# Performance work log

Measured on AMD Instinct MI355X. Metric: run time of the kernel, lower is better.

Reference implementation:

```python
import jax, jax.numpy as jnp
import numpy as np

# ---- model hyperparams (from init_kwargs) ----
N_USERS = 200000
N_ITEMS = 100000
DIM = 64
NNZ = 3000000
BATCH = 4096
N_HOPS = 3          # context_hops
EPS = 0.1           # SimGCL perturbation magnitude
TEMP = 0.2          # tau
CL_RATE = 0.5       # lamb
DECAY = 1e-4        # l2


def setup_inputs() -> dict:
    key = jax.random.key(0)
    k = jax.random.split(key, 8)
    user_embed = (jax.random.normal(k[0], (N_USERS, DIM), dtype=jnp.float32) * 0.01)
    item_embed = (jax.random.normal(k[1], (N_ITEMS, DIM), dtype=jnp.float32) * 0.01)
    N = N_USERS + N_ITEMS
    # COO normalized adjacency (buffer, not a parameter in the torch module)
    adj_rows = jax.random.randint(k[2], (NNZ,), 0, N)
    adj_cols = jax.random.randint(k[3], (NNZ,), 0, N)
    adj_vals = jax.random.uniform(k[4], (NNZ,), dtype=jnp.float32) * 0.2
    # unique index batches (torch code calls torch.unique for the CL loss;
    # sampling without replacement makes skipping unique exact, since the
    # InfoNCE mean is permutation invariant)
    users = jax.random.permutation(k[5], N_USERS)[:BATCH].astype(jnp.int32)
    pos_items = jax.random.permutation(k[6], N_ITEMS)[:BATCH].astype(jnp.int32)
    neg_items = jax.random.randint(k[7], (BATCH,), 0, N_ITEMS)
    return {"user_embed": user_embed, "item_embed": item_embed,
            "adj_vals": adj_vals, "adj_rows": adj_rows, "adj_cols": adj_cols,
            "users": users, "pos_items": pos_items, "neg_items": neg_items}


def _spmm(vals, rows, cols, x):
    # torch.sparse.mm(A, x) with A in COO form: out[r] += v * x[c]
    return jax.ops.segment_sum(vals[:, None] * x[cols], rows, num_segments=x.shape[0])


def _gcn(user_embed, item_embed, vals, rows, cols, perturbed, key):
    ego = jnp.concatenate([user_embed, item_embed], axis=0)  # [N, D]
    acc = jnp.zeros_like(ego)
    for h in range(N_HOPS):
        ego = _spmm(vals, rows, cols, ego)
        if perturbed:
            noise = jax.random.uniform(jax.random.fold_in(key, h), ego.shape, dtype=ego.dtype)
            noise = noise / jnp.maximum(jnp.linalg.norm(noise, axis=-1, keepdims=True), 1e-12)
            ego = ego + jnp.sign(ego) * noise * EPS
        acc = acc + ego
    mean = acc / N_HOPS   # stack + mean over hops == running-sum / n_hops
    return mean[:N_USERS], mean[N_USERS:]


def _info_nce(v1, v2, temp):
    v1 = v1 / jnp.maximum(jnp.linalg.norm(v1, axis=1, keepdims=True), 1e-12)
    v2 = v2 / jnp.maximum(jnp.linalg.norm(v2, axis=1, keepdims=True), 1e-12)
    pos = jnp.exp(jnp.sum(v1 * v2, axis=-1) / temp)              # [B]
    ttl = jnp.sum(jnp.exp((v1 @ v2.T) / temp), axis=1)           # [B]
    return jnp.mean(-jnp.log(pos / ttl + 1e-5))


def reference(user_embed, item_embed, adj_vals, adj_rows, adj_cols, users, pos_items, neg_items):
    # --- recommendation branch (no perturbation) ---
    ru, ri = _gcn(user_embed, item_embed, adj_vals, adj_rows, adj_cols, False, jax.random.key(0))
    ue, pe, ne = ru[users], ri[pos_items], ri[neg_items]
    pos_score = jnp.sum(ue * pe, axis=1)
    neg_score = jnp.sum(ue * ne, axis=1)
    rec_loss = jnp.mean(-jnp.log(1e-5 + jax.nn.sigmoid(pos_score - neg_score)))
    reg_loss = DECAY * (jnp.linalg.norm(ue) + jnp.linalg.norm(pe))  # Frobenius norms
    # --- contrastive branch: two perturbed views of the whole GCN ---
    u1, i1 = _gcn(user_embed, item_embed, adj_vals, adj_rows, adj_cols, True, jax.random.key(101))
    u2, i2 = _gcn(user_embed, item_embed, adj_vals, adj_rows, adj_cols, True, jax.random.key(202))
    cl_loss = CL_RATE * (_info_nce(u1[users], u2[users], TEMP)
                         + _info_nce(i1[pos_items], i2[pos_items], TEMP))
    return rec_loss + reg_loss + cl_loss
```

## Files before the change

kernel.cpp:

```cpp
#include <hip/hip_runtime.h>
#include <stdint.h>

#define NUSERS  200000
#define NITEMS  100000
#define NTOT    300000
#define DIM     64
#define NU64    (NUSERS * DIM)
#define NNZC    3000000
#define BATCH   4096
#define B64     (BATCH * DIM)
#define EPSP    0.1f
#define INV_TEMP 5.0f
#define SCAN_ELEMS 1024
#define GELEMS ((size_t)7 * B64 + 2 * BATCH + 8)
#define BCAP   163840

#define BSHIFT 11
#define BROWS  (1 << BSHIFT)
#define NB     ((NTOT + BROWS - 1) / BROWS)
#define CHUNK  4096
#define NCHUNK ((NNZC + CHUNK - 1) / CHUNK)
#define NH     (NB * NCHUNK)
#define CASTB  ((NTOT * DIM) / 2048)
#define Z4V    (NTOT / 4)
#define Z4T    ((2 * BATCH + 8) / 4)
#define ZVB    ((Z4V + 511) / 512)
#define ZTB    ((Z4T + 511) / 512)
#define SCB    ((NTOT + 255) / 256)

typedef short bf16x8 __attribute__((ext_vector_type(8)));
typedef float f32x4  __attribute__((ext_vector_type(4)));

__device__ __forceinline__ float b2f(unsigned short h) {
  return __uint_as_float(((uint32_t)h) << 16);
}
__device__ __forceinline__ unsigned short f2b(float f) {
  uint32_t b = __float_as_uint(f);
  uint32_t r = b + 0x7FFFu + ((b >> 16) & 1u);
  return (unsigned short)(r >> 16);
}

__device__ __forceinline__ uint32_t mix32(uint32_t h) {
  h ^= h >> 16; h *= 0x85EBCA6Bu;
  h ^= h >> 13; h *= 0xC2B2AE35u;
  h ^= h >> 16;
  return h;
}
__device__ __forceinline__ uint32_t noise_key(uint32_t seed, uint32_t hop) {
  return mix32(seed * 0x9E3779B9u + hop * 0x85EBCA6Bu + 0x1BD11BDAu);
}
__device__ __forceinline__ float fast_unif(uint32_t key, uint32_t e) {
  uint32_t h = mix32(key + e * 0x9E3779B9u);
  return __uint_as_float((h >> 9) | 0x3F800000u) - 1.0f;
}
__device__ __forceinline__ float n_ss4(uint32_t key, uint32_t rq, float4& u) {
  uint32_t h = mix32(key + rq * 0x9E3779B9u);
  u.x = ((float)(h & 255u)         + 0.5f) * (1.0f / 256.0f);
  u.y = ((float)((h >> 8) & 255u)  + 0.5f) * (1.0f / 256.0f);
  u.z = ((float)((h >> 16) & 255u) + 0.5f) * (1.0f / 256.0f);
  u.w = ((float)(h >> 24)          + 0.5f) * (1.0f / 256.0f);
  return u.x * u.x + u.y * u.y + u.z * u.z + u.w * u.w;
}

__device__ __forceinline__ float sgnf(float a) {
  return (a > 0.f) ? 1.f : ((a < 0.f) ? -1.f : 0.f);
}

__global__ __launch_bounds__(256) void partA_cast(
    const int* __restrict__ rows, int* __restrict__ Hcnt,
    const float* __restrict__ uemb, const float* __restrict__ iemb,
    unsigned short* __restrict__ X0,
    int* __restrict__ vflag, float* __restrict__ ttlz,
    float* __restrict__ sc1, float* __restrict__ sc2) {
  int blk = blockIdx.x;
  if (blk >= NCHUNK + CASTB + ZVB + ZTB) {
    int r = (blk - (NCHUNK + CASTB + ZVB + ZTB)) * 256 + threadIdx.x;
    if (r >= NTOT) return;
    const uint32_t k101 = noise_key(101u, 0u);
    const uint32_t k202 = noise_key(202u, 0u);
    float s1 = 0.f, s2 = 0.f;
    for (int q = 0; q < 16; ++q) {
      float4 u;
      s1 += n_ss4(k101, (uint32_t)(r * 16 + q), u);
      s2 += n_ss4(k202, (uint32_t)(r * 16 + q), u);
    }
    sc1[r] = EPSP / fmaxf(sqrtf(s1), 1e-12f);
    sc2[r] = EPSP / fmaxf(sqrtf(s2), 1e-12f);
    return;
  }
  if (blk >= NCHUNK + CASTB + ZVB) {
    int i4 = (blk - NCHUNK - CASTB - ZVB) * 512 + threadIdx.x;
    float4 z = make_float4(0.f, 0.f, 0.f, 0.f);
    if (i4 < Z4T) ((float4*)ttlz)[i4] = z;
    i4 += 256;
    if (i4 < Z4T) ((float4*)ttlz)[i4] = z;
    return;
  }
  if (blk >= NCHUNK + CASTB) {
    int i4 = (blk - NCHUNK - CASTB) * 512 + threadIdx.x;
    int4 z = make_int4(0, 0, 0, 0);
    if (i4 < Z4V) ((int4*)vflag)[i4] = z;
    i4 += 256;
    if (i4 < Z4V) ((int4*)vflag)[i4] = z;
    return;
  }
  if (blk >= NCHUNK) {
    int base = (blk - NCHUNK) * 2048 + threadIdx.x * 8;
    const float* src = (base < NU64) ? (uemb + base) : (iemb + (base - NU64));
    float4 f0 = ((const float4*)src)[0];
    float4 f1 = ((const float4*)src)[1];
    uint4 o;
    o.x = ((uint32_t)f2b(f0.y) << 16) | f2b(f0.x);
    o.y = ((uint32_t)f2b(f0.w) << 16) | f2b(f0.z);
    o.z = ((uint32_t)f2b(f1.y) << 16) | f2b(f1.x);
    o.w = ((uint32_t)f2b(f1.w) << 16) | f2b(f1.z);
    *(uint4*)(X0 + base) = o;
    return;
  }
  __shared__ int bc[256];
  int c = blk, t = threadIdx.x;
  bc[t] = 0;
  __syncthreads();
  int base = c * CHUNK;
  for (int i = t; i < CHUNK; i += 256) {
    int e = base + i;
    if (e < NNZC) atomicAdd(&bc[rows[e] >> BSHIFT], 1);
  }
  __syncthreads();
  if (t < NB) Hcnt[t * NCHUNK + c] = bc[t];
}

__global__ void scan_block(const int* __restrict__ cnt, int* __restrict__ out,
                           int* __restrict__ bsums, int n) {
  __shared__ int tmp[SCAN_ELEMS];
  int base = blockIdx.x * SCAN_ELEMS;
  int t = threadIdx.x;
  #pragma unroll
  for (int q = 0; q < 4; ++q) {
    int k = t + q * 256, i = base + k;
    tmp[k] = (i < n) ? cnt[i] : 0;
  }
  __syncthreads();
  for (int off = 1; off < SCAN_ELEMS; off <<= 1) {
    int v[4];
    #pragma unroll
    for (int q = 0; q < 4; ++q) {
      int k = t + q * 256;
      v[q] = (k >= off) ? tmp[k - off] : 0;
    }
    __syncthreads();
    #pragma unroll
    for (int q = 0; q < 4; ++q) tmp[t + q * 256] += v[q];
    __syncthreads();
  }
  #pragma unroll
  for (int q = 0; q < 4; ++q) {
    int k = t + q * 256, i = base + k;
    if (i < n) out[i] = (k == 0) ? 0 : tmp[k - 1];
  }
  if (t == 0) bsums[blockIdx.x] = tmp[SCAN_ELEMS - 1];
}

__global__ void add_offsets_scan(int* __restrict__ out,
                                 const int* __restrict__ bsums,
                                 int n, int nb) {
  __shared__ int tmp[512];
  int t = threadIdx.x;
  tmp[t] = (t < nb) ? bsums[t] : 0;
  tmp[t + 256] = (t + 256 < nb) ? bsums[t + 256] : 0;
  __syncthreads();
  for (int off = 1; off < 512; off <<= 1) {
    int v0 = (t >= off) ? tmp[t - off] : 0;
    int v1 = (t + 256 >= off) ? tmp[t + 256 - off] : 0;
    __syncthreads();
    tmp[t] += v0; tmp[t + 256] += v1;
    __syncthreads();
  }
  int i = blockIdx.x * 256 + t;
  if (i < n) {
    int b = i >> 10;
    out[i] += (b == 0) ? 0 : tmp[b - 1];
  }
}

__global__ void add_offsets_emit_scan(int* __restrict__ vmap,
                                      const int* __restrict__ bsums,
                                      const int* __restrict__ vflag,
                                      int* __restrict__ vlist,
                                      int* __restrict__ nV, int nb) {
  __shared__ int tmp[512];
  int t = threadIdx.x;
  tmp[t] = (t < nb) ? bsums[t] : 0;
  tmp[t + 256] = (t + 256 < nb) ? bsums[t + 256] : 0;
  __syncthreads();
  for (int off = 1; off < 512; off <<= 1) {
    int v0 = (t >= off) ? tmp[t - off] : 0;
    int v1 = (t + 256 >= off) ? tmp[t + 256 - off] : 0;
    __syncthreads();
    tmp[t] += v0; tmp[t + 256] += v1;
    __syncthreads();
  }
  int i = blockIdx.x * 256 + t;
  if (i >= NTOT) return;
  int b = i >> 10;
  int m = vmap[i] + ((b == 0) ? 0 : tmp[b - 1]);
  vmap[i] = m;
  if (vflag[i] && m < BCAP) vlist[m] = i;
  if (i == NTOT - 1) {
    int tot = m + vflag[i];
    nV[0] = (tot > BCAP) ? BCAP : tot;
  }
}

__global__ __launch_bounds__(256) void partB(const float* __restrict__ vals,
                                             const int* __restrict__ rows,
                                             const int* __restrict__ cols,
                                             const int* __restrict__ Hofs,
                                             int2* __restrict__ midp,
                                             int* __restrict__ midr) {
  __shared__ int2 stv[CHUNK];
  __shared__ int  str_[CHUNK];
  __shared__ int  cnt[256];
  __shared__ int  sc[256];
  __shared__ int  adj[NB];
  int c = blockIdx.x, t = threadIdx.x;
  cnt[t] = 0;
  __syncthreads();
  int base = c * CHUNK;
  for (int i = t; i < CHUNK; i += 256) {
    int e = base + i;
    if (e < NNZC) atomicAdd(&cnt[rows[e] >> BSHIFT], 1);
  }
  __syncthreads();
  sc[t] = cnt[t];
  __syncthreads();
  for (int off = 1; off < 256; off <<= 1) {
    int u = (t >= off) ? sc[t - off] : 0;
    __syncthreads();
    sc[t] += u;
    __syncthreads();
  }
  int excl = sc[t] - cnt[t];
  cnt[t] = excl;
  if (t < NB) adj[t] = Hofs[t * NCHUNK + c] - excl;
  __syncthreads();
  for (int i = t; i < CHUNK; i += 256) {
    int e = base + i;
    if (e < NNZC) {
      int r = rows[e];
      int b = r >> BSHIFT;
      int p = atomicAdd(&cnt[b], 1);
      stv[p] = make_int2(__float_as_int(vals[e]), cols[e] * DIM);
      str_[p] = r;
    }
  }
  __syncthreads();
  int n = NNZC - base;
  if (n > CHUNK) n = CHUNK;
  for (int p = t; p < n; p += 256) {
    int r = str_[p];
    int b = r >> BSHIFT;
    int dst = adj[b] + p;
    midp[dst] = stv[p];
    midr[dst] = r;
  }
}

__global__ __launch_bounds__(256) void partC(const int2* __restrict__ midp,
                                             const int* __restrict__ midr,
                                             const int* __restrict__ Hofs,
                                             int* __restrict__ rs,
                                             int2* __restrict__ pairs) {
  __shared__ int h[BROWS];
  __shared__ int tsum[256];
  int b = blockIdx.x, t = threadIdx.x;
  int row0 = b << BSHIFT;
  for (int i = t; i < BROWS; i += 256) h[i] = 0;
  __syncthreads();
  int s = Hofs[b * NCHUNK];
  int e = (b + 1 < NB) ? Hofs[(b + 1) * NCHUNK] : NNZC;
  for (int p = s + t; p < e; p += 256)
    atomicAdd(&h[midr[p] - row0], 1);
  __syncthreads();
  int loc[8], run = 0;
  #pragma unroll
  for (int k = 0; k < 8; ++k) { loc[k] = run; run += h[t * 8 + k]; }
  tsum[t] = run;
  __syncthreads();
  for (int off = 1; off < 256; off <<= 1) {
    int v = (t >= off) ? tsum[t - off] : 0;
    __syncthreads();
    tsum[t] += v;
    __syncthreads();
  }
  int baseT = (t == 0) ? 0 : tsum[t - 1];
  #pragma unroll
  for (int k = 0; k < 8; ++k) {
    int i = t * 8 + k;
    int pos = s + baseT + loc[k];
    if (row0 + i < NTOT) rs[row0 + i] = pos;
    h[i] = pos;
  }
  if (b == NB - 1 && t == 0) rs[NTOT] = NNZC;
  __syncthreads();
  for (int p = s + t; p < e; p += 256) {
    int r = midr[p];
    int2 v = midp[p];
    int pos = atomicAdd(&h[r - row0], 1);
    pairs[pos] = v;
  }
}

__global__ __launch_bounds__(256) void mark_v(const int* __restrict__ u,
                                              const int* __restrict__ p,
                                              const int* __restrict__ n,
                                              const int* __restrict__ rs,
                                              const int2* __restrict__ pairs,
                                              int* __restrict__ vflag) {
  int i = blockIdx.x * 256 + threadIdx.x;
  if (i >= 3 * BATCH) return;
  int v = (i < BATCH) ? u[i]
        : (i < 2 * BATCH) ? (NUSERS + p[i - BATCH])
        : (NUSERS + n[i - 2 * BATCH]);
  vflag[v] = 1;
  int s = rs[v], e = rs[v + 1];
  for (int j = s; j < e; ++j) vflag[(unsigned)pairs[j].y >> 6] = 1;
}

__global__ __launch_bounds__(256) void spmm_hop0(
    const int2* __restrict__ pairs, const int* __restrict__ rs,
    const unsigned short* __restrict__ x,
    unsigned short* __restrict__ y) {
  int tid  = threadIdx.x;
  int lane = tid & 63;
  int q    = lane & 15;
  int wave = (blockIdx.x * 256 + tid) >> 6;
  int r    = wave * 4 + (lane >> 4);
  int s    = rs[r];
  int e    = rs[r + 1];
  int q4 = q * 4;
  float a0[4] = {0.f, 0.f, 0.f, 0.f};
  for (int j = s; j < e; j += 8) {
    int2 p[8];
    #pragma unroll
    for (int k = 0; k < 8; ++k)
      p[k] = (j + k < e) ? pairs[j + k] : make_int2(0, 0);
    #pragma unroll
    for (int k = 0; k < 8; ++k) {
      float v = __int_as_float(p[k].x);
      unsigned o = (unsigned)(p[k].y + q4);
      ushort4 h = *(const ushort4*)(x + o);
      a0[0] = fmaf(v, b2f(h.x), a0[0]); a0[1] = fmaf(v, b2f(h.y), a0[1]);
      a0[2] = fmaf(v, b2f(h.z), a0[2]); a0[3] = fmaf(v, b2f(h.w), a0[3]);
    }
  }
  int ebase = r * 64 + q4;
  ushort4 st;
  st.x = f2b(a0[0]); st.y = f2b(a0[1]); st.z = f2b(a0[2]); st.w = f2b(a0[3]);
  *(ushort4*)(y + ebase) = st;
}

__global__ __launch_bounds__(256) void spmm_subz(
    const int2* __restrict__ pairs, const int* __restrict__ rs,
    const int* __restrict__ vlist, const int* __restrict__ nVp,
    const unsigned short* __restrict__ A,
    const float* __restrict__ sc1, const float* __restrict__ sc2,
    unsigned short* __restrict__ y0, unsigned short* __restrict__ y1,
    unsigned short* __restrict__ y2) {
  int nV = nVp[0];
  int z  = blockIdx.x % 3;
  int bx = blockIdx.x / 3;
  if (bx * 16 >= nV) return;
  unsigned short* y = (z == 0) ? y0 : ((z == 1) ? y1 : y2);
  const float* scg = (z == 1) ? sc1 : sc2;
  int tid  = threadIdx.x;
  int lane = tid & 63;
  int q    = lane & 15;
  int wave = (bx * 256 + tid) >> 6;
  int slot = wave * 4 + (lane >> 4);
  if (slot >= nV) return;
  int v = vlist[slot];
  int s = rs[v];
  int e = rs[v + 1];
  int q4 = q * 4;
  float a0[4] = {0.f, 0.f, 0.f, 0.f};
  if (z == 0) {
    for (int j = s; j < e; j += 8) {
      int2 p[8];
      #pragma unroll
      for (int k = 0; k < 8; ++k)
        p[k] = (j + k < e) ? pairs[j + k] : make_int2(0, 0);
      #pragma unroll
      for (int k = 0; k < 8; ++k) {
        float vv = __int_as_float(p[k].x);
        unsigned o = (unsigned)(p[k].y + q4);
        ushort4 h = *(const ushort4*)(A + o);
        a0[0] = fmaf(vv, b2f(h.x), a0[0]); a0[1] = fmaf(vv, b2f(h.y), a0[1]);
        a0[2] = fmaf(vv, b2f(h.z), a0[2]); a0[3] = fmaf(vv, b2f(h.w), a0[3]);
      }
    }
  } else {
    const uint32_t kg = noise_key((z == 1) ? 101u : 202u, 0u);
    for (int j = s; j < e; j += 8) {
      int2 p[8];
      #pragma unroll
      for (int k = 0; k < 8; ++k)
        p[k] = (j + k < e) ? pairs[j + k] : make_int2(0, 0);
      #pragma unroll
      for (int k = 0; k < 8; ++k) {
        float vv = __int_as_float(p[k].x);
        unsigned o = (unsigned)(p[k].y + q4);
        ushort4 h = *(const ushort4*)(A + o);
        float sc = scg[(unsigned)p[k].y >> 6];
        float4 u;
        n_ss4(kg, ((unsigned)p[k].y >> 2) + (unsigned)q, u);
        float a_ = b2f(h.x), b_ = b2f(h.y), c_ = b2f(h.z), d_ = b2f(h.w);
        a0[0] = fmaf(vv, fmaf(sgnf(a_) * u.x, sc, a_), a0[0]);
        a0[1] = fmaf(vv, fmaf(sgnf(b_) * u.y, sc, b_), a0[1]);
        a0[2] = fmaf(vv, fmaf(sgnf(c_) * u.z, sc, c_), a0[2]);
        a0[3] = fmaf(vv, fmaf(sgnf(d_) * u.w, sc, d_), a0[3]);
      }
    }
    uint32_t key = noise_key((z == 1) ? 101u : 202u, 1u);
    int en = v * 64 + q4;
    float u[4], ss = 0.f;
    #pragma unroll
    for (int k = 0; k < 4; ++k) {
      u[k] = fast_unif(key, (uint32_t)(en + k));
      ss += u[k] * u[k];
    }
    #pragma unroll
    for (int msk = 1; msk < 16; msk <<= 1) ss += __shfl_xor(ss, msk);
    float sc = EPSP / fmaxf(sqrtf(ss), 1e-12f);
    #pragma unroll
    for (int k = 0; k < 4; ++k) a0[k] += sgnf(a0[k]) * u[k] * sc;
  }
  ushort4 st;
  st.x = f2b(a0[0]); st.y = f2b(a0[1]); st.z = f2b(a0[2]); st.w = f2b(a0[3]);
  *(ushort4*)(y + slot * 64 + q4) = st;
}

__global__ __launch_bounds__(256) void hop2g7(
    const int2* __restrict__ pairs, const int* __restrict__ rs,
    const unsigned short* __restrict__ Abuf,
    const unsigned short* __restrict__ B0,
    const unsigned short* __restrict__ B1,
    const unsigned short* __restrict__ B2,
    const int* __restrict__ vmap,
    const float* __restrict__ sc1, const float* __restrict__ sc2,
    const int* __restrict__ users, const int* __restrict__ pos,
    const int* __restrict__ neg,
    float* __restrict__ g, unsigned short* __restrict__ gb) {
  int by = blockIdx.y;
  int br = (by < 3) ? 0 : ((by < 5) ? 1 : 2);
  const int* idx = (by == 2) ? neg
                 : ((by == 1 || by == 4 || by == 6) ? pos : users);
  int base = (by == 0 || by == 3 || by == 5) ? 0 : NUSERS;
  float* o = g + (size_t)by * B64;
  const unsigned short* Bt = (br == 0) ? B0 : ((br == 1) ? B1 : B2);
  uint32_t seed = (br == 1) ? 101u : 202u;
  int tid  = threadIdx.x;
  int lane = tid & 63;
  int q    = lane & 15;
  int q4 = q * 4;
  int slot = blockIdx.x * 16 + (tid >> 6) * 4 + (lane >> 4);
  int row  = base + idx[slot];
  int s    = rs[row];
  int e    = rs[row + 1];
  float a0[4] = {0.f, 0.f, 0.f, 0.f};
  for (int j = s; j < e; j += 8) {
    int2 p[8];
    #pragma unroll
    for (int k = 0; k < 8; ++k)
      p[k] = (j + k < e) ? pairs[j + k] : make_int2(0, 0);
    int sl[8];
    #pragma unroll
    for (int k = 0; k < 8; ++k)
      sl[k] = vmap[(unsigned)p[k].y >> 6];
    #pragma unroll
    for (int k = 0; k < 8; ++k) {
      float v = __int_as_float(p[k].x);
      unsigned of = (unsigned)(sl[k] * DIM + q4);
      ushort4 h = *(const ushort4*)(Bt + of);
      a0[0] = fmaf(v, b2f(h.x), a0[0]); a0[1] = fmaf(v, b2f(h.y), a0[1]);
      a0[2] = fmaf(v, b2f(h.z), a0[2]); a0[3] = fmaf(v, b2f(h.w), a0[3]);
    }
  }
  if (br) {
    uint32_t key = noise_key(seed, 2u);
    int en = row * 64 + q4;
    float u[4], ss = 0.f;
    #pragma unroll
    for (int k = 0; k < 4; ++k) {
      u[k] = fast_unif(key, (uint32_t)(en + k));
      ss += u[k] * u[k];
    }
    #pragma unroll
    for (int msk = 1; msk < 16; msk <<= 1) ss += __shfl_xor(ss, msk);
    float sc = EPSP / fmaxf(sqrtf(ss), 1e-12f);
    #pragma unroll
    for (int k = 0; k < 4; ++k) a0[k] += sgnf(a0[k]) * u[k] * sc;
  }
  size_t rbA = (size_t)row * DIM + q4;
  size_t rbB = (size_t)vmap[row] * DIM + q4;
  ushort4 ha = *(const ushort4*)(Abuf + rbA);
  ushort4 hb = *(const ushort4*)(Bt + rbB);
  float af[4] = {b2f(ha.x), b2f(ha.y), b2f(ha.z), b2f(ha.w)};
  if (br) {
    uint32_t key0 = noise_key(seed, 0u);
    float scn = ((br == 1) ? sc1 : sc2)[row];
    float4 u;
    n_ss4(key0, (uint32_t)(row * 16 + q), u);
    af[0] = fmaf(sgnf(af[0]) * u.x, scn, af[0]);
    af[1] = fmaf(sgnf(af[1]) * u.y, scn, af[1]);
    af[2] = fmaf(sgnf(af[2]) * u.z, scn, af[2]);
    af[3] = fmaf(sgnf(af[3]) * u.w, scn, af[3]);
  }
  float rv[4];
  rv[0] = (af[0] + b2f(hb.x)) + a0[0];
  rv[1] = (af[1] + b2f(hb.y)) + a0[1];
  rv[2] = (af[2] + b2f(hb.z)) + a0[2];
  rv[3] = (af[3] + b2f(hb.w)) + a0[3];
  if (br) {
    float ss = rv[0]*rv[0] + rv[1]*rv[1] + rv[2]*rv[2] + rv[3]*rv[3];
    #pragma unroll
    for (int msk = 1; msk < 16; msk <<= 1) ss += __shfl_xor(ss, msk);
    float inv = 1.0f / fmaxf(sqrtf(ss), 1e-12f);
    #pragma unroll
    for (int k = 0; k < 4; ++k) rv[k] *= inv;
  }
  int og = slot * 64 + q4;
  *(float4*)(o + og) = make_float4(rv[0], rv[1], rv[2], rv[3]);
  if (br) {
    unsigned short* ob = gb + (size_t)(by - 3) * B64;
    ushort4 sb;
    sb.x = f2b(rv[0]); sb.y = f2b(rv[1]); sb.z = f2b(rv[2]); sb.w = f2b(rv[3]);
    *(ushort4*)(ob + og) = sb;
  }
}

__global__ __launch_bounds__(256) void nce_ttl_mfma(
    const unsigned short* __restrict__ u1b, const unsigned short* __restrict__ u2b,
    float* __restrict__ tu,
    const unsigned short* __restrict__ w1b, const unsigned short* __restrict__ w2b,
    float* __restrict__ tw) {
  const unsigned short* V1 = (blockIdx.z == 0) ? u1b : w1b;
  const unsigned short* V2 = (blockIdx.z == 0) ? u2b : w2b;
  float* ttl = (blockIdx.z == 0) ? tu : tw;
  int tid  = threadIdx.x;
  int lane = tid & 63;
  int wv   = tid >> 6;
  int lr   = lane & 15;
  int lk   = (lane >> 4) * 8;
  int m0   = blockIdx.x * 64 + wv * 16;
  bf16x8 a0 = *(const bf16x8*)(V1 + (size_t)(m0 + lr) * DIM + lk);
  bf16x8 a1 = *(const bf16x8*)(V1 + (size_t)(m0 + lr) * DIM + 32 + lk);
  float rowsum[4] = {0.f, 0.f, 0.f, 0.f};
  int n0 = blockIdx.y * 256;
  for (int ch = 0; ch < 4; ++ch) {
    int nc = n0 + ch * 64;
    #pragma unroll
    for (int nt = 0; nt < 4; ++nt) {
      int col = nc + nt * 16 + lr;
      bf16x8 b0 = *(const bf16x8*)(V2 + (size_t)col * DIM + lk);
      bf16x8 b1 = *(const bf16x8*)(V2 + (size_t)col * DIM + 32 + lk);
      f32x4 c = {0.f, 0.f, 0.f, 0.f};
      c = __builtin_amdgcn_mfma_f32_16x16x32_bf16(a0, b0, c, 0, 0, 0);
      c = __builtin_amdgcn_mfma_f32_16x16x32_bf16(a1, b1, c, 0, 0, 0);
      #pragma unroll
      for (int rr = 0; rr < 4; ++rr)
        rowsum[rr] += __expf(c[rr] * INV_TEMP);
    }
  }
  #pragma unroll
  for (int rr = 0; rr < 4; ++rr) {
    float s = rowsum[rr];
    #pragma unroll
    for (int m = 1; m < 16; m <<= 1) s += __shfl_xor(s, m);
    rowsum[rr] = s;
  }
  if (lr == 0) {
    int rbase = m0 + (lane >> 4) * 4;
    #pragma unroll
    for (int rr = 0; rr < 4; ++rr)
      atomicAdd(&ttl[rbase + rr], rowsum[rr]);
  }
}

__global__ __launch_bounds__(256) void loss3(const float* __restrict__ g,
                                             const float* __restrict__ ttl_u,
                                             float* __restrict__ acc) {
  __shared__ float red[3][4];
  int role = blockIdx.y;
  int tid = threadIdx.x, lane = tid & 63, wv = tid >> 6;
  int gw = blockIdx.x * 4 + wv;
  if (role == 0) {
    const float* ue = g;
    const float* pe = g + (size_t)B64;
    const float* ne = g + 2 * (size_t)B64;
    const float third = 1.0f / 3.0f;
    float l = 0.f, su = 0.f, sp = 0.f;
    for (int r = gw; r < BATCH; r += 256) {
      int gid = r * 64 + lane;
      float u = ue[gid] * third, p = pe[gid] * third, n = ne[gid] * third;
      float ps = u * p, ns = u * n;
      su += u * u; sp += p * p;
      #pragma unroll
      for (int m = 32; m; m >>= 1) { ps += __shfl_xor(ps, m); ns += __shfl_xor(ns, m); }
      if (lane == 0) {
        float sig = 1.0f / (1.0f + __expf(-(ps - ns)));
        l += -logf(1e-5f + sig);
      }
    }
    #pragma unroll
    for (int m = 32; m; m >>= 1) { su += __shfl_xor(su, m); sp += __shfl_xor(sp, m); }
    if (lane == 0) { red[0][wv] = l; red[1][wv] = su; red[2][wv] = sp; }
    __syncthreads();
    if (tid == 0) {
      atomicAdd(acc + 0, red[0][0] + red[0][1] + red[0][2] + red[0][3]);
      atomicAdd(acc + 1, red[1][0] + red[1][1] + red[1][2] + red[1][3]);
      atomicAdd(acc + 2, red[2][0] + red[2][1] + red[2][2] + red[2][3]);
    }
  } else {
    int by = role - 1;
    const float* v1 = g + (size_t)(3 + by) * B64;
    const float* v2 = g + (size_t)(5 + by) * B64;
    const float* ttl = ttl_u + by * BATCH;
    float l = 0.f;
    for (int r = gw; r < BATCH; r += 256) {
      int gid = r * 64 + lane;
      float p = v1[gid] * v2[gid];
      #pragma unroll
      for (int m = 32; m; m >>= 1) p += __shfl_xor(p, m);
      if (lane == 0) l += -logf(__expf(p * INV_TEMP) / ttl[r] + 1e-5f);
    }
    if (lane == 0) red[0][wv] = l;
    __syncthreads();
    if (tid == 0)
      atomicAdd(acc + 3 + by, red[0][0] + red[0][1] + red[0][2] + red[0][3]);
  }
}

__global__ void finalize_kernel(const float* __restrict__ acc, float* __restrict__ out) {
  out[0] = acc[0] * (1.0f / BATCH)
         + 1e-4f * (sqrtf(acc[1]) + sqrtf(acc[2]))
         + 0.5f * (acc[3] + acc[4]) * (1.0f / BATCH);
}

extern "C" void kernel_launch(void* const* d_in, const int* in_sizes, int n_in,
                              void* d_out, int out_size, void* d_ws, size_t ws_size,
                              hipStream_t stream) {
  (void)in_sizes; (void)n_in; (void)out_size; (void)ws_size;
  const float* user_embed = (const float*)d_in[0];
  const float* item_embed = (const float*)d_in[1];
  const float* adj_vals   = (const float*)d_in[2];
  const int*   adj_rows   = (const int*)d_in[3];
  const int*   adj_cols   = (const int*)d_in[4];
  const int*   users      = (const int*)d_in[5];
  const int*   pos_items  = (const int*)d_in[6];
  const int*   neg_items  = (const int*)d_in[7];
  float* out = (float*)d_out;

  const size_t bufElems = (size_t)NTOT * DIM;
  const size_t bcapE    = (size_t)BCAP * DIM;

  unsigned short* A  = (unsigned short*)d_ws;
  unsigned short* B0 = A + bufElems;
  unsigned short* B1 = B0 + bcapE;
  unsigned short* B2 = B1 + bcapE;
  float* sc1 = (float*)(B2 + bcapE);
  float* sc2 = sc1 + NTOT;
  int2*  pairs = (int2*)(sc2 + NTOT);
  float* g     = (float*)(pairs + NNZC);
  int*   rs    = (int*)(g + GELEMS);
  int*   bsums = rs + (NTOT + 4);
  int*   vflag = bsums + 512;
  int*   vmap  = vflag + NTOT;
  int*   vlist = vmap + NTOT;
  int*   nVd   = vlist + NTOT;
  unsigned short* gb =
      (unsigned short*)(((uintptr_t)(nVd + 1) + 31) & ~(uintptr_t)31);

  float* ttl_u = g + 7 * (size_t)B64;
  float* ttl_i = ttl_u + BATCH;
  float* acc   = ttl_u + 2 * BATCH;
  unsigned short* g_u1b = gb + 0 * (size_t)B64;
  unsigned short* g_i1b = gb + 1 * (size_t)B64;
  unsigned short* g_u2b = gb + 2 * (size_t)B64;
  unsigned short* g_i2b = gb + 3 * (size_t)B64;

  int2* midp = (int2*)A;
  int*  midr = (int*)(midp + NNZC);
  int*  Hcnt = midr + NNZC;
  int*  Hofs = Hcnt + NH;
  unsigned short* X0 = B0;

  partA_cast<<<NCHUNK + CASTB + ZVB + ZTB + SCB, 256, 0, stream>>>(
      adj_rows, Hcnt, user_embed, item_embed, X0, vflag, ttl_u, sc1, sc2);
  const int nhb = (NH + SCAN_ELEMS - 1) / SCAN_ELEMS;
  scan_block<<<nhb, 256, 0, stream>>>(Hcnt, Hofs, bsums, NH);
  add_offsets_scan<<<(NH + 255) / 256, 256, 0, stream>>>(Hofs, bsums, NH, nhb);
  partB<<<NCHUNK, 256, 0, stream>>>(adj_vals, adj_rows, adj_cols, Hofs, midp, midr);
  partC<<<NB, 256, 0, stream>>>(midp, midr, Hofs, rs, pairs);

  mark_v<<<(3 * BATCH + 255) / 256, 256, 0, stream>>>(
      users, pos_items, neg_items, rs, pairs, vflag);
  const int nvb = (NTOT + SCAN_ELEMS - 1) / SCAN_ELEMS;
  scan_block<<<nvb, 256, 0, stream>>>(vflag, vmap, bsums, NTOT);
  add_offsets_emit_scan<<<(NTOT + 255) / 256, 256, 0, stream>>>(
      vmap, bsums, vflag, vlist, nVd, nvb);

  const int spmm_blocks = NTOT / 16;

  spmm_hop0<<<spmm_blocks, 256, 0, stream>>>(pairs, rs, X0, A);

  spmm_subz<<<3 * spmm_blocks, 256, 0, stream>>>(
      pairs, rs, vlist, nVd, A, sc1, sc2, B0, B1, B2);

  dim3 h2g7(BATCH / 16, 7);
  hop2g7<<<h2g7, 256, 0, stream>>>(pairs, rs, A, B0, B1, B2, vmap, sc1, sc2,
                                   users, pos_items, neg_items, g, gb);

  dim3 nce_grid(BATCH / 64, BATCH / 256, 2);
  nce_ttl_mfma<<<nce_grid, 256, 0, stream>>>(g_u1b, g_u2b, ttl_u,
                                             g_i1b, g_i2b, ttl_i);
  dim3 lgrid(64, 3);
  loss3<<<lgrid, 256, 0, stream>>>(g, ttl_u, acc);
  finalize_kernel<<<1, 1, 0, stream>>>(acc, out);
}
```

Measured before the change: 528.9 us.

## Precompute perturbed hop-1 views in hop0 and fuse three views per gather

The first-hop SpMM now also writes the two noise-perturbed copies of its output, with the noise norm computed by in-row shuffles, so the separate per-row norm-scale pass and the per-edge noise regeneration in hop 2 are removed. The hop-2 and hop-3 kernels then accumulate all three views in one pass over each row's edge list, sharing the index and value loads instead of launching a separate block set per view. The cost is two extra full-size bf16 buffers written and then gathered from at random, which adds memory traffic and register pressure.

```diff
diff --git a/kernel.cpp b/kernel.cpp
--- a/kernel.cpp
+++ b/kernel.cpp
@@ -26,7 +26,6 @@
 #define Z4T    ((2 * BATCH + 8) / 4)
 #define ZVB    ((Z4V + 511) / 512)
 #define ZTB    ((Z4T + 511) / 512)
-#define SCB    ((NTOT + 255) / 256)
 
 typedef short bf16x8 __attribute__((ext_vector_type(8)));
 typedef float f32x4  __attribute__((ext_vector_type(4)));
@@ -70,24 +69,8 @@
     const int* __restrict__ rows, int* __restrict__ Hcnt,
     const float* __restrict__ uemb, const float* __restrict__ iemb,
     unsigned short* __restrict__ X0,
-    int* __restrict__ vflag, float* __restrict__ ttlz,
-    float* __restrict__ sc1, float* __restrict__ sc2) {
+    int* __restrict__ vflag, float* __restrict__ ttlz) {
   int blk = blockIdx.x;
-  if (blk >= NCHUNK + CASTB + ZVB + ZTB) {
-    int r = (blk - (NCHUNK + CASTB + ZVB + ZTB)) * 256 + threadIdx.x;
-    if (r >= NTOT) return;
-    const uint32_t k101 = noise_key(101u, 0u);
-    const uint32_t k202 = noise_key(202u, 0u);
-    float s1 = 0.f, s2 = 0.f;
-    for (int q = 0; q < 16; ++q) {
-      float4 u;
-      s1 += n_ss4(k101, (uint32_t)(r * 16 + q), u);
-      s2 += n_ss4(k202, (uint32_t)(r * 16 + q), u);
-    }
-    sc1[r] = EPSP / fmaxf(sqrtf(s1), 1e-12f);
-    sc2[r] = EPSP / fmaxf(sqrtf(s2), 1e-12f);
-    return;
-  }
   if (blk >= NCHUNK + CASTB + ZVB) {
     int i4 = (blk - NCHUNK - CASTB - ZVB) * 512 + threadIdx.x;
     float4 z = make_float4(0.f, 0.f, 0.f, 0.f);
@@ -327,10 +310,13 @@
   for (int j = s; j < e; ++j) vflag[(unsigned)pairs[j].y >> 6] = 1;
 }
 
-__global__ __launch_bounds__(256) void spmm_hop0(
+__global__ __launch_bounds__(256) void spmm_hop3(
     const int2* __restrict__ pairs, const int* __restrict__ rs,
     const unsigned short* __restrict__ x,
-    unsigned short* __restrict__ y) {
+    unsigned short* __restrict__ A, unsigned short* __restrict__ A1,
+    unsigned short* __restrict__ A2) {
+  const uint32_t k101 = noise_key(101u, 0u);
+  const uint32_t k202 = noise_key(202u, 0u);
   int tid  = threadIdx.x;
   int lane = tid & 63;
   int q    = lane & 15;
@@ -357,72 +343,82 @@
   int ebase = r * 64 + q4;
   ushort4 st;
   st.x = f2b(a0[0]); st.y = f2b(a0[1]); st.z = f2b(a0[2]); st.w = f2b(a0[3]);
-  *(ushort4*)(y + ebase) = st;
-}
-
-__global__ __launch_bounds__(256) void spmm_subz(
+  *(ushort4*)(A + ebase) = st;
+  float a[4] = {b2f(st.x), b2f(st.y), b2f(st.z), b2f(st.w)};
+  float4 u1, u2;
+  float s1 = n_ss4(k101, (uint32_t)(r * 16 + q), u1);
+  float s2 = n_ss4(k202, (uint32_t)(r * 16 + q), u2);
+  #pragma unroll
+  for (int m = 1; m < 16; m <<= 1) {
+    s1 += __shfl_xor(s1, m);
+    s2 += __shfl_xor(s2, m);
+  }
+  float sc1 = EPSP / fmaxf(sqrtf(s1), 1e-12f);
+  float sc2 = EPSP / fmaxf(sqrtf(s2), 1e-12f);
+  float g0 = sgnf(a[0]), g1 = sgnf(a[1]), g2 = sgnf(a[2]), g3 = sgnf(a[3]);
+  ushort4 o1, o2;
+  o1.x = f2b(fmaf(g0 * u1.x, sc1, a[0]));
+  o1.y = f2b(fmaf(g1 * u1.y, sc1, a[1]));
+  o1.z = f2b(fmaf(g2 * u1.z, sc1, a[2]));
+  o1.w = f2b(fmaf(g3 * u1.w, sc1, a[3]));
+  o2.x = f2b(fmaf(g0 * u2.x, sc2, a[0]));
+  o2.y = f2b(fmaf(g1 * u2.y, sc2, a[1]));
+  o2.z = f2b(fmaf(g2 * u2.z, sc2, a[2]));
+  o2.w = f2b(fmaf(g3 * u2.w, sc2, a[3]));
+  *(ushort4*)(A1 + ebase) = o1;
+  *(ushort4*)(A2 + ebase) = o2;
+}
+
+__global__ __launch_bounds__(256) void spmm_sub3t(
     const int2* __restrict__ pairs, const int* __restrict__ rs,
     const int* __restrict__ vlist, const int* __restrict__ nVp,
     const unsigned short* __restrict__ A,
-    const float* __restrict__ sc1, const float* __restrict__ sc2,
+    const unsigned short* __restrict__ A1,
+    const unsigned short* __restrict__ A2,
     unsigned short* __restrict__ y0, unsigned short* __restrict__ y1,
     unsigned short* __restrict__ y2) {
   int nV = nVp[0];
-  int z  = blockIdx.x % 3;
-  int bx = blockIdx.x / 3;
-  if (bx * 16 >= nV) return;
-  unsigned short* y = (z == 0) ? y0 : ((z == 1) ? y1 : y2);
-  const float* scg = (z == 1) ? sc1 : sc2;
+  if (blockIdx.x * 16 >= nV) return;
   int tid  = threadIdx.x;
   int lane = tid & 63;
   int q    = lane & 15;
-  int wave = (bx * 256 + tid) >> 6;
+  int wave = (blockIdx.x * 256 + tid) >> 6;
   int slot = wave * 4 + (lane >> 4);
   if (slot >= nV) return;
   int v = vlist[slot];
   int s = rs[v];
   int e = rs[v + 1];
   int q4 = q * 4;
-  float a0[4] = {0.f, 0.f, 0.f, 0.f};
-  if (z == 0) {
-    for (int j = s; j < e; j += 8) {
-      int2 p[8];
-      #pragma unroll
-      for (int k = 0; k < 8; ++k)
-        p[k] = (j + k < e) ? pairs[j + k] : make_int2(0, 0);
-      #pragma unroll
-      for (int k = 0; k < 8; ++k) {
-        float vv = __int_as_float(p[k].x);
-        unsigned o = (unsigned)(p[k].y + q4);
-        ushort4 h = *(const ushort4*)(A + o);
-        a0[0] = fmaf(vv, b2f(h.x), a0[0]); a0[1] = fmaf(vv, b2f(h.y), a0[1]);
-        a0[2] = fmaf(vv, b2f(h.z), a0[2]); a0[3] = fmaf(vv, b2f(h.w), a0[3]);
-      }
-    }
-  } else {
-    const uint32_t kg = noise_key((z == 1) ? 101u : 202u, 0u);
-    for (int j = s; j < e; j += 8) {
-      int2 p[8];
-      #pragma unroll
-      for (int k = 0; k < 8; ++k)
-        p[k] = (j + k < e) ? pairs[j + k] : make_int2(0, 0);
-      #pragma unroll
-      for (int k = 0; k < 8; ++k) {
-        float vv = __int_as_float(p[k].x);
-        unsigned o = (unsigned)(p[k].y + q4);
-        ushort4 h = *(const ushort4*)(A + o);
-        float sc = scg[(unsigned)p[k].y >> 6];
-        float4 u;
-        n_ss4(kg, ((unsigned)p[k].y >> 2) + (unsigned)q, u);
-        float a_ = b2f(h.x), b_ = b2f(h.y), c_ = b2f(h.z), d_ = b2f(h.w);
-        a0[0] = fmaf(vv, fmaf(sgnf(a_) * u.x, sc, a_), a0[0]);
-        a0[1] = fmaf(vv, fmaf(sgnf(b_) * u.y, sc, b_), a0[1]);
-        a0[2] = fmaf(vv, fmaf(sgnf(c_) * u.z, sc, c_), a0[2]);
-        a0[3] = fmaf(vv, fmaf(sgnf(d_) * u.w, sc, d_), a0[3]);
-      }
-    }
-    uint32_t key = noise_key((z == 1) ? 101u : 202u, 1u);
-    int en = v * 64 + q4;
+  float c0[4] = {0,0,0,0}, c1[4] = {0,0,0,0}, c2[4] = {0,0,0,0};
+  for (int j = s; j < e; j += 8) {
+    int2 p[8];
+    #pragma unroll
+    for (int k = 0; k < 8; ++k)
+      p[k] = (j + k < e) ? pairs[j + k] : make_int2(0, 0);
+    #pragma unroll
+    for (int k = 0; k < 8; ++k) {
+      float vv = __int_as_float(p[k].x);
+      unsigned o = (unsigned)(p[k].y + q4);
+      ushort4 h0 = *(const ushort4*)(A  + o);
+      ushort4 h1 = *(const ushort4*)(A1 + o);
+      ushort4 h2 = *(const ushort4*)(A2 + o);
+      c0[0] = fmaf(vv, b2f(h0.x), c0[0]); c0[1] = fmaf(vv, b2f(h0.y), c0[1]);
+      c0[2] = fmaf(vv, b2f(h0.z), c0[2]); c0[3] = fmaf(vv, b2f(h0.w), c0[3]);
+      c1[0] = fmaf(vv, b2f(h1.x), c1[0]); c1[1] = fmaf(vv, b2f(h1.y), c1[1]);
+      c1[2] = fmaf(vv, b2f(h1.z), c1[2]); c1[3] = fmaf(vv, b2f(h1.w), c1[3]);
+      c2[0] = fmaf(vv, b2f(h2.x), c2[0]); c2[1] = fmaf(vv, b2f(h2.y), c2[1]);
+      c2[2] = fmaf(vv, b2f(h2.z), c2[2]); c2[3] = fmaf(vv, b2f(h2.w), c2[3]);
+    }
+  }
+  int ob = slot * 64 + q4;
+  int en = v * 64 + q4;
+  {
+    ushort4 st;
+    st.x = f2b(c0[0]); st.y = f2b(c0[1]); st.z = f2b(c0[2]); st.w = f2b(c0[3]);
+    *(ushort4*)(y0 + ob) = st;
+  }
+  {
+    uint32_t key = noise_key(101u, 1u);
     float u[4], ss = 0.f;
     #pragma unroll
     for (int k = 0; k < 4; ++k) {
@@ -433,32 +429,43 @@
     for (int msk = 1; msk < 16; msk <<= 1) ss += __shfl_xor(ss, msk);
     float sc = EPSP / fmaxf(sqrtf(ss), 1e-12f);
     #pragma unroll
-    for (int k = 0; k < 4; ++k) a0[k] += sgnf(a0[k]) * u[k] * sc;
-  }
-  ushort4 st;
-  st.x = f2b(a0[0]); st.y = f2b(a0[1]); st.z = f2b(a0[2]); st.w = f2b(a0[3]);
-  *(ushort4*)(y + slot * 64 + q4) = st;
-}
-
-__global__ __launch_bounds__(256) void hop2g7(
+    for (int k = 0; k < 4; ++k) c1[k] += sgnf(c1[k]) * u[k] * sc;
+    ushort4 st;
+    st.x = f2b(c1[0]); st.y = f2b(c1[1]); st.z = f2b(c1[2]); st.w = f2b(c1[3]);
+    *(ushort4*)(y1 + ob) = st;
+  }
+  {
+    uint32_t key = noise_key(202u, 1u);
+    float u[4], ss = 0.f;
+    #pragma unroll
+    for (int k = 0; k < 4; ++k) {
+      u[k] = fast_unif(key, (uint32_t)(en + k));
+      ss += u[k] * u[k];
+    }
+    #pragma unroll
+    for (int msk = 1; msk < 16; msk <<= 1) ss += __shfl_xor(ss, msk);
+    float sc = EPSP / fmaxf(sqrtf(ss), 1e-12f);
+    #pragma unroll
+    for (int k = 0; k < 4; ++k) c2[k] += sgnf(c2[k]) * u[k] * sc;
+    ushort4 st;
+    st.x = f2b(c2[0]); st.y = f2b(c2[1]); st.z = f2b(c2[2]); st.w = f2b(c2[3]);
+    *(ushort4*)(y2 + ob) = st;
+  }
+}
+
+__global__ __launch_bounds__(256) void hop2g3(
     const int2* __restrict__ pairs, const int* __restrict__ rs,
     const unsigned short* __restrict__ Abuf,
     const unsigned short* __restrict__ B0,
     const unsigned short* __restrict__ B1,
     const unsigned short* __restrict__ B2,
     const int* __restrict__ vmap,
-    const float* __restrict__ sc1, const float* __restrict__ sc2,
     const int* __restrict__ users, const int* __restrict__ pos,
     const int* __restrict__ neg,
     float* __restrict__ g, unsigned short* __restrict__ gb) {
-  int by = blockIdx.y;
-  int br = (by < 3) ? 0 : ((by < 5) ? 1 : 2);
-  const int* idx = (by == 2) ? neg
-                 : ((by == 1 || by == 4 || by == 6) ? pos : users);
-  int base = (by == 0 || by == 3 || by == 5) ? 0 : NUSERS;
-  float* o = g + (size_t)by * B64;
-  const unsigned short* Bt = (br == 0) ? B0 : ((br == 1) ? B1 : B2);
-  uint32_t seed = (br == 1) ? 101u : 202u;
+  int seg = blockIdx.y;
+  const int* idx = (seg == 0) ? users : ((seg == 1) ? pos : neg);
+  int base = (seg == 0) ? 0 : NUSERS;
   int tid  = threadIdx.x;
   int lane = tid & 63;
   int q    = lane & 15;
@@ -467,7 +474,8 @@
   int row  = base + idx[slot];
   int s    = rs[row];
   int e    = rs[row + 1];
-  float a0[4] = {0.f, 0.f, 0.f, 0.f};
+  bool all3 = (seg < 2);
+  float a0[4] = {0,0,0,0}, a1[4] = {0,0,0,0}, a2[4] = {0,0,0,0};
   for (int j = s; j < e; j += 8) {
     int2 p[8];
     #pragma unroll
@@ -481,58 +489,86 @@
     for (int k = 0; k < 8; ++k) {
       float v = __int_as_float(p[k].x);
       unsigned of = (unsigned)(sl[k] * DIM + q4);
-      ushort4 h = *(const ushort4*)(Bt + of);
-      a0[0] = fmaf(v, b2f(h.x), a0[0]); a0[1] = fmaf(v, b2f(h.y), a0[1]);
-      a0[2] = fmaf(v, b2f(h.z), a0[2]); a0[3] = fmaf(v, b2f(h.w), a0[3]);
-    }
-  }
-  if (br) {
-    uint32_t key = noise_key(seed, 2u);
-    int en = row * 64 + q4;
-    float u[4], ss = 0.f;
-    #pragma unroll
-    for (int k = 0; k < 4; ++k) {
-      u[k] = fast_unif(key, (uint32_t)(en + k));
-      ss += u[k] * u[k];
-    }
-    #pragma unroll
-    for (int msk = 1; msk < 16; msk <<= 1) ss += __shfl_xor(ss, msk);
-    float sc = EPSP / fmaxf(sqrtf(ss), 1e-12f);
-    #pragma unroll
-    for (int k = 0; k < 4; ++k) a0[k] += sgnf(a0[k]) * u[k] * sc;
+      ushort4 h0 = *(const ushort4*)(B0 + of);
+      a0[0] = fmaf(v, b2f(h0.x), a0[0]); a0[1] = fmaf(v, b2f(h0.y), a0[1]);
+      a0[2] = fmaf(v, b2f(h0.z), a0[2]); a0[3] = fmaf(v, b2f(h0.w), a0[3]);
+      if (all3) {
+        ushort4 h1 = *(const ushort4*)(B1 + of);
+        ushort4 h2 = *(const ushort4*)(B2 + of);
+        a1[0] = fmaf(v, b2f(h1.x), a1[0]); a1[1] = fmaf(v, b2f(h1.y), a1[1]);
+        a1[2] = fmaf(v, b2f(h1.z), a1[2]); a1[3] = fmaf(v, b2f(h1.w), a1[3]);
+        a2[0] = fmaf(v, b2f(h2.x), a2[0]); a2[1] = fmaf(v, b2f(h2.y), a2[1]);
+        a2[2] = fmaf(v, b2f(h2.z), a2[2]); a2[3] = fmaf(v, b2f(h2.w), a2[3]);
+      }
+    }
   }
   size_t rbA = (size_t)row * DIM + q4;
   size_t rbB = (size_t)vmap[row] * DIM + q4;
   ushort4 ha = *(const ushort4*)(Abuf + rbA);
-  ushort4 hb = *(const ushort4*)(Bt + rbB);
-  float af[4] = {b2f(ha.x), b2f(ha.y), b2f(ha.z), b2f(ha.w)};
-  if (br) {
-    uint32_t key0 = noise_key(seed, 0u);
-    float scn = ((br == 1) ? sc1 : sc2)[row];
-    float4 u;
-    n_ss4(key0, (uint32_t)(row * 16 + q), u);
-    af[0] = fmaf(sgnf(af[0]) * u.x, scn, af[0]);
-    af[1] = fmaf(sgnf(af[1]) * u.y, scn, af[1]);
-    af[2] = fmaf(sgnf(af[2]) * u.z, scn, af[2]);
-    af[3] = fmaf(sgnf(af[3]) * u.w, scn, af[3]);
-  }
-  float rv[4];
-  rv[0] = (af[0] + b2f(hb.x)) + a0[0];
-  rv[1] = (af[1] + b2f(hb.y)) + a0[1];
-  rv[2] = (af[2] + b2f(hb.z)) + a0[2];
-  rv[3] = (af[3] + b2f(hb.w)) + a0[3];
-  if (br) {
-    float ss = rv[0]*rv[0] + rv[1]*rv[1] + rv[2]*rv[2] + rv[3]*rv[3];
-    #pragma unroll
-    for (int msk = 1; msk < 16; msk <<= 1) ss += __shfl_xor(ss, msk);
-    float inv = 1.0f / fmaxf(sqrtf(ss), 1e-12f);
-    #pragma unroll
-    for (int k = 0; k < 4; ++k) rv[k] *= inv;
-  }
-  int og = slot * 64 + q4;
-  *(float4*)(o + og) = make_float4(rv[0], rv[1], rv[2], rv[3]);
-  if (br) {
-    unsigned short* ob = gb + (size_t)(by - 3) * B64;
+  float af0 = b2f(ha.x), af1 = b2f(ha.y), af2 = b2f(ha.z), af3 = b2f(ha.w);
+  {
+    ushort4 hb = *(const ushort4*)(B0 + rbB);
+    float rv[4];
+    rv[0] = (af0 + b2f(hb.x)) + a0[0];
+    rv[1] = (af1 + b2f(hb.y)) + a0[1];
+    rv[2] = (af2 + b2f(hb.z)) + a0[2];
+    rv[3] = (af3 + b2f(hb.w)) + a0[3];
+    int og = slot * 64 + q4;
+    float* o = g + (size_t)seg * B64;
+    *(float4*)(o + og) = make_float4(rv[0], rv[1], rv[2], rv[3]);
+  }
+  if (!all3) return;
+  #pragma unroll
+  for (int br = 1; br <= 2; ++br) {
+    uint32_t seed = (br == 1) ? 101u : 202u;
+    float* ab = (br == 1) ? a1 : a2;
+    const unsigned short* Bt = (br == 1) ? B1 : B2;
+    {
+      uint32_t key = noise_key(seed, 2u);
+      int en = row * 64 + q4;
+      float u[4], ss = 0.f;
+      #pragma unroll
+      for (int k = 0; k < 4; ++k) {
+        u[k] = fast_unif(key, (uint32_t)(en + k));
+        ss += u[k] * u[k];
+      }
+      #pragma unroll
+      for (int msk = 1; msk < 16; msk <<= 1) ss += __shfl_xor(ss, msk);
+      float sc = EPSP / fmaxf(sqrtf(ss), 1e-12f);
+      #pragma unroll
+      for (int k = 0; k < 4; ++k) ab[k] += sgnf(ab[k]) * u[k] * sc;
+    }
+    float af[4] = {af0, af1, af2, af3};
+    {
+      uint32_t key0 = noise_key(seed, 0u);
+      float4 u;
+      float ssn = n_ss4(key0, (uint32_t)(row * 16 + q), u);
+      #pragma unroll
+      for (int m = 1; m < 16; m <<= 1) ssn += __shfl_xor(ssn, m);
+      float scn = EPSP / fmaxf(sqrtf(ssn), 1e-12f);
+      af[0] = fmaf(sgnf(af[0]) * u.x, scn, af[0]);
+      af[1] = fmaf(sgnf(af[1]) * u.y, scn, af[1]);
+      af[2] = fmaf(sgnf(af[2]) * u.z, scn, af[2]);
+      af[3] = fmaf(sgnf(af[3]) * u.w, scn, af[3]);
+    }
+    ushort4 hb = *(const ushort4*)(Bt + rbB);
+    float rv[4];
+    rv[0] = (af[0] + b2f(hb.x)) + ab[0];
+    rv[1] = (af[1] + b2f(hb.y)) + ab[1];
+    rv[2] = (af[2] + b2f(hb.z)) + ab[2];
+    rv[3] = (af[3] + b2f(hb.w)) + ab[3];
+    {
+      float ss = rv[0]*rv[0] + rv[1]*rv[1] + rv[2]*rv[2] + rv[3]*rv[3];
+      #pragma unroll
+      for (int msk = 1; msk < 16; msk <<= 1) ss += __shfl_xor(ss, msk);
+      float inv = 1.0f / fmaxf(sqrtf(ss), 1e-12f);
+      #pragma unroll
+      for (int k = 0; k < 4; ++k) rv[k] *= inv;
+    }
+    int og = slot * 64 + q4;
+    float* o = g + (size_t)(3 + (br - 1) * 2 + seg) * B64;
+    *(float4*)(o + og) = make_float4(rv[0], rv[1], rv[2], rv[3]);
+    unsigned short* ob = gb + (size_t)((br - 1) * 2 + seg) * B64;
     ushort4 sb;
     sb.x = f2b(rv[0]); sb.y = f2b(rv[1]); sb.z = f2b(rv[2]); sb.w = f2b(rv[3]);
     *(ushort4*)(ob + og) = sb;
@@ -665,12 +701,12 @@
   const size_t bcapE    = (size_t)BCAP * DIM;
 
   unsigned short* A  = (unsigned short*)d_ws;
-  unsigned short* B0 = A + bufElems;
+  unsigned short* A1 = A + bufElems;
+  unsigned short* A2 = A1 + bufElems;
+  unsigned short* B0 = A2 + bufElems;
   unsigned short* B1 = B0 + bcapE;
   unsigned short* B2 = B1 + bcapE;
-  float* sc1 = (float*)(B2 + bcapE);
-  float* sc2 = sc1 + NTOT;
-  int2*  pairs = (int2*)(sc2 + NTOT);
+  int2*  pairs = (int2*)(B2 + bcapE);
   float* g     = (float*)(pairs + NNZC);
   int*   rs    = (int*)(g + GELEMS);
   int*   bsums = rs + (NTOT + 4);
@@ -685,8 +721,8 @@
   float* ttl_i = ttl_u + BATCH;
   float* acc   = ttl_u + 2 * BATCH;
   unsigned short* g_u1b = gb + 0 * (size_t)B64;
+  unsigned short* g_u2b = gb + 2 * (size_t)B64;
   unsigned short* g_i1b = gb + 1 * (size_t)B64;
-  unsigned short* g_u2b = gb + 2 * (size_t)B64;
   unsigned short* g_i2b = gb + 3 * (size_t)B64;
 
   int2* midp = (int2*)A;
@@ -695,8 +731,8 @@
   int*  Hofs = Hcnt + NH;
   unsigned short* X0 = B0;
 
-  partA_cast<<<NCHUNK + CASTB + ZVB + ZTB + SCB, 256, 0, stream>>>(
-      adj_rows, Hcnt, user_embed, item_embed, X0, vflag, ttl_u, sc1, sc2);
+  partA_cast<<<NCHUNK + CASTB + ZVB + ZTB, 256, 0, stream>>>(
+      adj_rows, Hcnt, user_embed, item_embed, X0, vflag, ttl_u);
   const int nhb = (NH + SCAN_ELEMS - 1) / SCAN_ELEMS;
   scan_block<<<nhb, 256, 0, stream>>>(Hcnt, Hofs, bsums, NH);
   add_offsets_scan<<<(NH + 255) / 256, 256, 0, stream>>>(Hofs, bsums, NH, nhb);
@@ -712,13 +748,13 @@
 
   const int spmm_blocks = NTOT / 16;
 
-  spmm_hop0<<<spmm_blocks, 256, 0, stream>>>(pairs, rs, X0, A);
-
-  spmm_subz<<<3 * spmm_blocks, 256, 0, stream>>>(
-      pairs, rs, vlist, nVd, A, sc1, sc2, B0, B1, B2);
-
-  dim3 h2g7(BATCH / 16, 7);
-  hop2g7<<<h2g7, 256, 0, stream>>>(pairs, rs, A, B0, B1, B2, vmap, sc1, sc2,
+  spmm_hop3<<<spmm_blocks, 256, 0, stream>>>(pairs, rs, X0, A, A1, A2);
+
+  spmm_sub3t<<<spmm_blocks, 256, 0, stream>>>(pairs, rs, vlist, nVd,
+                                              A, A1, A2, B0, B1, B2);
+
+  dim3 h2g3(BATCH / 16, 3);
+  hop2g3<<<h2g3, 256, 0, stream>>>(pairs, rs, A, B0, B1, B2, vmap,
                                    users, pos_items, neg_items, g, gb);
 
   dim3 nce_grid(BATCH / 64, BATCH / 256, 2);
```

New measurement: 485.3 us. -8.2%, faster.
